# Performance work log

Hardware: AMD Instinct MI355X
Metric: run time of the kernel (lower is better)

## Reference

```python
import jax, jax.numpy as jnp
import numpy as np

NSAMPLE = 1024   # FPS centroids S
NGROUP = 32      # neighbors per ball K
RADIUS = 0.2


def _sqdist(a, b):
    # a: [B,S,3], b: [B,N,3] -> [B,S,N] squared euclidean distances
    return (jnp.sum(a * a, -1)[:, :, None]
            + jnp.sum(b * b, -1)[:, None, :]
            - 2.0 * jnp.einsum('bsc,bnc->bsn', a, b))


def farthest_point_sample(xyz, npoint):
    # xyz: [B,N,3] -> indices [B,npoint]. Deterministic start at index 0
    # (torch version randomizes the first centroid).
    B, N, _ = xyz.shape

    def step(carry, _):
        distance, farthest = carry
        centroid = jnp.take_along_axis(xyz, farthest[:, None, None], axis=1)  # [B,1,3]
        d = jnp.sum((xyz - centroid) ** 2, -1)                                 # [B,N]
        distance = jnp.minimum(distance, d)
        new_far = jnp.argmax(distance, -1).astype(jnp.int32)
        return (distance, new_far), farthest

    init = (jnp.full((B, N), 1e10, xyz.dtype), jnp.zeros((B,), jnp.int32))
    _, cents = jax.lax.scan(step, init, None, length=npoint)  # [npoint,B]
    return cents.T  # [B,npoint]


def query_ball_point(radius, nsample, xyz, new_xyz):
    # xyz: [B,N,3], new_xyz: [B,S,3] -> int idx [B,S,nsample]
    B, N, _ = xyz.shape
    sqr = _sqdist(new_xyz, xyz)                       # [B,S,N]
    idx = jnp.broadcast_to(jnp.arange(N, dtype=jnp.int32), sqr.shape)
    idx = jnp.where(sqr > radius * radius, N, idx)    # invalid -> sentinel N
    idx = jnp.sort(idx, axis=-1)[:, :, :nsample]      # smallest valid indices first
    first = idx[:, :, :1]
    idx = jnp.where(idx == N, first, idx)             # pad with first neighbor
    return idx.astype(jnp.int32)


def _gather_points(points, idx):
    # points: [B,N,C], idx: [B,S,K] -> [B,S,K,C]
    return jax.vmap(lambda p, i: p[i])(points, idx)


def setup_inputs() -> dict:
    key = jax.random.key(0)
    ks = jax.random.split(key, 8)
    B, N, D = 16, 8192, 64
    xyz = jax.random.uniform(ks[0], (B, N, 3), dtype=jnp.float32)
    points_fea = jax.random.normal(ks[1], (B, N, D), dtype=jnp.float32)
    s = 0.05
    W1 = jax.random.normal(ks[2], (67, 64), dtype=jnp.float32) * s
    b1 = jnp.zeros((64,), jnp.float32)
    W2 = jax.random.normal(ks[3], (64, 128), dtype=jnp.float32) * s
    b2 = jnp.zeros((128,), jnp.float32)
    W3 = jax.random.normal(ks[4], (128, 256), dtype=jnp.float32) * s
    b3 = jnp.zeros((256,), jnp.float32)
    return {"xyz": xyz, "points_fea": points_fea, "W1": W1, "b1": b1,
            "W2": W2, "b2": b2, "W3": W3, "b3": b3}


def reference(xyz, points_fea, W1, b1, W2, b2, W3, b3):
    # --- sample_and_group (fps + ball query) ---
    fps_idx = farthest_point_sample(xyz, NSAMPLE)                       # [B,S]
    sampled_xyz = jnp.take_along_axis(xyz, fps_idx[..., None], axis=1)  # [B,S,3]
    grouped_idx = query_ball_point(RADIUS, NGROUP, xyz, sampled_xyz)    # [B,S,K]
    grouped_xyz = _gather_points(xyz, grouped_idx)                      # [B,S,K,3]
    rel = grouped_xyz - sampled_xyz[:, :, None, :]
    grouped_fea = _gather_points(points_fea, grouped_idx)               # [B,S,K,D]
    feats = jnp.concatenate([rel, grouped_fea], axis=-1)                # [B,S,K,3+D]
    # --- per-point MLP (Linear+ReLU x3) ---
    h = jax.nn.relu(feats @ W1 + b1)
    h = jax.nn.relu(h @ W2 + b2)
    h = jax.nn.relu(h @ W3 + b3)                                        # [B,S,K,256]
    # --- max-pool over neighbors ---
    out = jnp.max(h, axis=2)                                            # [B,S,256]
    return sampled_xyz, out
```

## Files before the change

### kernel.cpp

```cpp
#include <hip/hip_runtime.h>
#include <hip/hip_bf16.h>

#define N_PTS 8192
#define NSAMP 1024
#define NGRP  32

typedef __attribute__((ext_vector_type(8))) short bf16x8;
typedef __attribute__((ext_vector_type(4))) float f32x4;

static __device__ inline unsigned short f2bf(float f) {
  __hip_bfloat16 h = __float2bfloat16(f);
  return __builtin_bit_cast(unsigned short, h);
}

#define DPP_MAXSTEP(r, ctrl)                                                  \
  r = fmaxf(r, __int_as_float(__builtin_amdgcn_update_dpp(                    \
          __float_as_int(r), __float_as_int(r), (ctrl), 0xf, 0xf, false)))

__global__
__attribute__((amdgpu_flat_work_group_size(512, 512)))
__attribute__((amdgpu_waves_per_eu(2, 2)))
void fps_kernel(
    const float* __restrict__ xyz, float* __restrict__ out_sampled)
{
  #pragma clang fp contract(off)
  const int b = blockIdx.x;
  const int t = threadIdx.x;
  const float* bx = xyz + (size_t)b * N_PTS * 3;

  float px[16], py[16], pz[16], dist[16];
  {
    const float4* src = (const float4*)(bx + t * 48);
    float4 v0 = src[0], v1 = src[1], v2 = src[2];
    float4 v3 = src[3], v4 = src[4], v5 = src[5];
    float4 v6 = src[6], v7 = src[7], v8 = src[8];
    float4 v9 = src[9], v10 = src[10], v11 = src[11];
    px[ 0]=v0.x; py[ 0]=v0.y; pz[ 0]=v0.z;
    px[ 1]=v0.w; py[ 1]=v1.x; pz[ 1]=v1.y;
    px[ 2]=v1.z; py[ 2]=v1.w; pz[ 2]=v2.x;
    px[ 3]=v2.y; py[ 3]=v2.z; pz[ 3]=v2.w;
    px[ 4]=v3.x; py[ 4]=v3.y; pz[ 4]=v3.z;
    px[ 5]=v3.w; py[ 5]=v4.x; pz[ 5]=v4.y;
    px[ 6]=v4.z; py[ 6]=v4.w; pz[ 6]=v5.x;
    px[ 7]=v5.y; py[ 7]=v5.z; pz[ 7]=v5.w;
    px[ 8]=v6.x; py[ 8]=v6.y; pz[ 8]=v6.z;
    px[ 9]=v6.w; py[ 9]=v7.x; pz[ 9]=v7.y;
    px[10]=v7.z; py[10]=v7.w; pz[10]=v8.x;
    px[11]=v8.y; py[11]=v8.z; pz[11]=v8.w;
    px[12]=v9.x; py[12]=v9.y; pz[12]=v9.z;
    px[13]=v9.w; py[13]=v10.x; pz[13]=v10.y;
    px[14]=v10.z; py[14]=v10.w; pz[14]=v11.x;
    px[15]=v11.y; py[15]=v11.z; pz[15]=v11.w;
  }
  #pragma unroll
  for (int r = 0; r < 16; ++r) dist[r] = 10000000000.0f;

  __shared__ uint2 part[2][8];
  __shared__ float out_lds[NSAMP * 3];

  const int lane = t & 63;
  const int wv   = t >> 6;

  float cx = bx[0], cy = bx[1], cz = bx[2];

  for (int it = 0; it < NSAMP; ++it) {
    if (t == 0) {
      out_lds[it * 3 + 0] = cx;
      out_lds[it * 3 + 1] = cy;
      out_lds[it * 3 + 2] = cz;
    }

    float bv = -1.0f;
    #pragma unroll
    for (int r = 0; r < 16; ++r) {
      float dx = px[r] - cx;
      float dy = py[r] - cy;
      float dz = pz[r] - cz;
      float d  = fmaf(dz, dz, fmaf(dy, dy, dx * dx));
      float nd = fminf(dist[r], d);
      dist[r] = nd;
      bv = fmaxf(bv, nd);
    }
    int bi = t * 16 + 15;
    #pragma unroll
    for (int r = 14; r >= 0; --r) bi = (dist[r] == bv) ? (t * 16 + r) : bi;

    float rmax = bv;
    DPP_MAXSTEP(rmax, 0x111);
    DPP_MAXSTEP(rmax, 0x112);
    DPP_MAXSTEP(rmax, 0x114);
    DPP_MAXSTEP(rmax, 0x118);
    DPP_MAXSTEP(rmax, 0x142);
    DPP_MAXSTEP(rmax, 0x143);
    float vmax = __int_as_float(
        __builtin_amdgcn_readlane(__float_as_int(rmax), 63));

    unsigned long long m = __ballot(bv == vmax);
    int L = __ffsll((long long)m) - 1;
    int widx = __builtin_amdgcn_readlane(bi, L);

    const int slot = it & 1;
    if (lane == 0) part[slot][wv] = make_uint2(__float_as_uint(vmax), (unsigned)widx);
    __syncthreads();

    const uint4* pp = (const uint4*)&part[slot][0];
    uint4 p0 = pp[0], p1 = pp[1], p2 = pp[2], p3 = pp[3];
    float v = __uint_as_float(p0.x); unsigned f = p0.y;
    float w1v = __uint_as_float(p0.z);
    if (w1v > v) { v = w1v; f = p0.w; }
    float w2v = __uint_as_float(p1.x);
    if (w2v > v) { v = w2v; f = p1.y; }
    float w3v = __uint_as_float(p1.z);
    if (w3v > v) { v = w3v; f = p1.w; }
    float w4v = __uint_as_float(p2.x);
    if (w4v > v) { v = w4v; f = p2.y; }
    float w5v = __uint_as_float(p2.z);
    if (w5v > v) { v = w5v; f = p2.w; }
    float w6v = __uint_as_float(p3.x);
    if (w6v > v) { v = w6v; f = p3.y; }
    float w7v = __uint_as_float(p3.z);
    if (w7v > v) { v = w7v; f = p3.w; }

    cx = bx[f * 3 + 0];
    cy = bx[f * 3 + 1];
    cz = bx[f * 3 + 2];
  }

  __syncthreads();
  float* ob = out_sampled + (size_t)b * NSAMP * 3;
  for (int i = t; i < NSAMP * 3; i += 512) ob[i] = out_lds[i];
}

__global__ __launch_bounds__(256) void ball_kernel(
    const float* __restrict__ xyz, const float* __restrict__ sampled,
    int* __restrict__ gidx)
{
  #pragma clang fp contract(off)
  const float R2 = (float)(0.2 * 0.2);
  int gt = blockIdx.x * 256 + threadIdx.x;
  int w = gt >> 6;
  int lane = gt & 63;
  const int b = w >> 10;
  const float* cp = sampled + (size_t)w * 3;
  float cx = cp[0], cy = cp[1], cz = cp[2];
  float na = ((cx * cx) + (cy * cy)) + (cz * cz);
  const float* bx = xyz + (size_t)b * N_PTS * 3;
  int* out = gidx + (size_t)w * NGRP;

  int cnt = 0;
  int first = 0;
  for (int base = 0; base < N_PTS && cnt < NGRP; base += 64) {
    int p = base + lane;
    float x = bx[p * 3 + 0];
    float y = bx[p * 3 + 1];
    float z = bx[p * 3 + 2];
    float nb  = ((x * x) + (y * y)) + (z * z);
    float dot = fmaf(cz, z, fmaf(cy, y, cx * x));
    float sq  = (na + nb) - (2.0f * dot);
    bool inr = !(sq > R2);
    unsigned long long m = __ballot(inr);
    if (cnt == 0 && m != 0ull) first = base + (__ffsll(m) - 1);
    int before = __popcll(m & ((1ull << lane) - 1ull));
    int pos = cnt + before;
    if (inr && pos < NGRP) out[pos] = p;
    cnt += __popcll(m);
  }
  if (cnt < NGRP) {
    int q = cnt + lane;
    if (q < NGRP) out[q] = first;
  }
}

__global__ __launch_bounds__(256) void prep_w_kernel(
    const float* __restrict__ W1, const float* __restrict__ W2,
    const float* __restrict__ W3, unsigned short* __restrict__ wf1,
    unsigned short* __restrict__ wf2, unsigned short* __restrict__ wf3)
{
  int tid = blockIdx.x * 256 + threadIdx.x;
  int rec = tid >> 6, lane = tid & 63;
  if (rec >= 92) return;
  const float* W; unsigned short* dst; int N, K, ksteps, rl;
  if (rec < 12)      { W = W1; dst = wf1; N = 64;  K = 67;  ksteps = 3; rl = rec; }
  else if (rec < 28) { W = W2; dst = wf2; N = 128; K = 64;  ksteps = 2; rl = rec - 12; }
  else               { W = W3; dst = wf3; N = 256; K = 128; ksteps = 4; rl = rec - 28; }
  int nt = rl / ksteps, ks = rl - nt * ksteps;
  int n  = nt * 16 + (lane & 15);
  int kb = ks * 32 + (lane >> 4) * 8;
  unsigned short v[8] __attribute__((aligned(16)));
  #pragma unroll
  for (int j = 0; j < 8; ++j) {
    int k = kb + j;
    v[j] = f2bf((k < K) ? W[k * N + n] : 0.0f);
  }
  *(uint4*)(dst + ((size_t)rl * 64 + lane) * 8) = *(const uint4*)v;
}

__global__ __launch_bounds__(256, 4) void mlp_mfma_kernel(
    const float* __restrict__ xyz, const float* __restrict__ fea,
    const float* __restrict__ sampled, const int* __restrict__ gidx,
    const unsigned short* __restrict__ wf1, const unsigned short* __restrict__ wf2,
    const unsigned short* __restrict__ wf3, const float* __restrict__ b1,
    const float* __restrict__ b2, const float* __restrict__ b3,
    float* __restrict__ out)
{
  __shared__ __align__(16) unsigned short fT[32][104];
  __shared__ __align__(16) unsigned short h1[32][72];
  __shared__ __align__(16) unsigned short h2[32][136];
  __shared__ float pmax[8][256];
  __shared__ int   sidx[32];
  __shared__ float sc[4];

  const int bs = blockIdx.x;
  const int b  = bs >> 10;
  const int t  = threadIdx.x;
  const int w    = t >> 6;
  const int lane = t & 63;
  const int quad = lane >> 4;
  const int ncol = lane & 15;

  if (t < 32) sidx[t] = gidx[(size_t)bs * 32 + t];
  if (t < 3)  sc[t] = sampled[(size_t)bs * 3 + t];
  __syncthreads();

  {
    const int pt = t >> 3, c0 = t & 7;
    const int p = sidx[pt];
    const float* xp = xyz + ((size_t)b * N_PTS + p) * 3;
    const float* fp = fea + ((size_t)b * N_PTS + p) * 64;
    for (int c = c0; c < 96; c += 8) {
      float v = (c < 3) ? (xp[c] - sc[c]) : (c < 67 ? fp[c - 3] : 0.0f);
      fT[pt][c] = f2bf(v);
    }
  }
  __syncthreads();

  #pragma unroll
  for (int q2 = 0; q2 < 2; ++q2) {
    const int tid = w * 2 + q2, mt = tid & 1, nt = tid >> 1;
    float bb = b1[nt * 16 + ncol];
    f32x4 acc = {bb, bb, bb, bb};
    #pragma unroll
    for (int ks = 0; ks < 3; ++ks) {
      bf16x8 a = *(const bf16x8*)&fT[mt * 16 + ncol][ks * 32 + quad * 8];
      bf16x8 bf = *(const bf16x8*)(wf1 + ((size_t)(nt * 3 + ks) * 64 + lane) * 8);
      acc = __builtin_amdgcn_mfma_f32_16x16x32_bf16(a, bf, acc, 0, 0, 0);
    }
    #pragma unroll
    for (int r = 0; r < 4; ++r)
      h1[mt * 16 + quad * 4 + r][nt * 16 + ncol] = f2bf(fmaxf(acc[r], 0.0f));
  }
  __syncthreads();

  #pragma unroll
  for (int q2 = 0; q2 < 4; ++q2) {
    const int tid = w * 4 + q2, mt = tid & 1, nt = tid >> 1;
    float bb = b2[nt * 16 + ncol];
    f32x4 acc = {bb, bb, bb, bb};
    #pragma unroll
    for (int ks = 0; ks < 2; ++ks) {
      bf16x8 a = *(const bf16x8*)&h1[mt * 16 + ncol][ks * 32 + quad * 8];
      bf16x8 bf = *(const bf16x8*)(wf2 + ((size_t)(nt * 2 + ks) * 64 + lane) * 8);
      acc = __builtin_amdgcn_mfma_f32_16x16x32_bf16(a, bf, acc, 0, 0, 0);
    }
    #pragma unroll
    for (int r = 0; r < 4; ++r)
      h2[mt * 16 + quad * 4 + r][nt * 16 + ncol] = f2bf(fmaxf(acc[r], 0.0f));
  }
  __syncthreads();

  #pragma unroll
  for (int q2 = 0; q2 < 8; ++q2) {
    const int tid = w * 8 + q2, mt = tid & 1, nt = tid >> 1;
    float bb = b3[nt * 16 + ncol];
    f32x4 acc = {bb, bb, bb, bb};
    #pragma unroll
    for (int ks = 0; ks < 4; ++ks) {
      bf16x8 a = *(const bf16x8*)&h2[mt * 16 + ncol][ks * 32 + quad * 8];
      bf16x8 bf = *(const bf16x8*)(wf3 + ((size_t)(nt * 4 + ks) * 64 + lane) * 8);
      acc = __builtin_amdgcn_mfma_f32_16x16x32_bf16(a, bf, acc, 0, 0, 0);
    }
    float mx = fmaxf(fmaxf(acc[0], acc[1]), fmaxf(acc[2], acc[3]));
    pmax[mt * 4 + quad][nt * 16 + ncol] = mx;
  }
  __syncthreads();

  {
    float v = pmax[0][t];
    #pragma unroll
    for (int s = 1; s < 8; ++s) v = fmaxf(v, pmax[s][t]);
    out[(size_t)bs * 256 + t] = fmaxf(v, 0.0f);
  }
}

extern "C" void kernel_launch(void* const* d_in, const int* in_sizes, int n_in,
                              void* d_out, int out_size, void* d_ws, size_t ws_size,
                              hipStream_t stream) {
  const float* xyz = (const float*)d_in[0];
  const float* fea = (const float*)d_in[1];
  const float* W1  = (const float*)d_in[2];
  const float* b1  = (const float*)d_in[3];
  const float* W2  = (const float*)d_in[4];
  const float* b2  = (const float*)d_in[5];
  const float* W3  = (const float*)d_in[6];
  const float* b3  = (const float*)d_in[7];

  float* outp    = (float*)d_out;
  float* sampled = outp;
  float* mlp_out = outp + 16 * 1024 * 3;
  int*   gidx    = (int*)d_ws;
  unsigned short* wf1 = (unsigned short*)((char*)d_ws + (2u << 20));
  unsigned short* wf2 = wf1 + (size_t)12 * 64 * 8;
  unsigned short* wf3 = wf2 + (size_t)16 * 64 * 8;

  fps_kernel<<<16, 512, 0, stream>>>(xyz, sampled);
  prep_w_kernel<<<23, 256, 0, stream>>>(W1, W2, W3, wf1, wf2, wf3);
  ball_kernel<<<4096, 256, 0, stream>>>(xyz, sampled, gidx);
  mlp_mfma_kernel<<<16384, 256, 0, stream>>>(xyz, fea, sampled, gidx,
                                             wf1, wf2, wf3, b1, b2, b3, mlp_out);
}
```

Before: 1.096 ms.

## Fuse FPS, ball query and MLP into one persistent producer-consumer kernel

Merges the three kernels into one persistent launch. Sixteen blocks run farthest point sampling and publish centroids in chunks of 64 through atomic counters, while the remaining blocks pull tasks from an atomic work queue, spin-wait until their centroid is ready, then do the ball query in one wave and the MLP. The aim is to overlap the serial FPS phase with grouping and MLP work and to drop the gidx round trip through global memory and the separate launches. In exchange it relies on co-residency of all 256 blocks to avoid deadlock, adds spin-wait and atomic overhead, and leaves only 240 consumer blocks of 512 threads doing the MLP.

```diff
diff --git a/kernel.cpp b/kernel.cpp
--- a/kernel.cpp
+++ b/kernel.cpp
@@ -4,6 +4,7 @@
 #define N_PTS 8192
 #define NSAMP 1024
 #define NGRP  32
+#define NTASK (16 * NSAMP)
 
 typedef __attribute__((ext_vector_type(8))) short bf16x8;
 typedef __attribute__((ext_vector_type(4))) float f32x4;
@@ -16,160 +17,6 @@
 #define DPP_MAXSTEP(r, ctrl)                                                  \
   r = fmaxf(r, __int_as_float(__builtin_amdgcn_update_dpp(                    \
           __float_as_int(r), __float_as_int(r), (ctrl), 0xf, 0xf, false)))
-
-__global__
-__attribute__((amdgpu_flat_work_group_size(512, 512)))
-__attribute__((amdgpu_waves_per_eu(2, 2)))
-void fps_kernel(
-    const float* __restrict__ xyz, float* __restrict__ out_sampled)
-{
-  #pragma clang fp contract(off)
-  const int b = blockIdx.x;
-  const int t = threadIdx.x;
-  const float* bx = xyz + (size_t)b * N_PTS * 3;
-
-  float px[16], py[16], pz[16], dist[16];
-  {
-    const float4* src = (const float4*)(bx + t * 48);
-    float4 v0 = src[0], v1 = src[1], v2 = src[2];
-    float4 v3 = src[3], v4 = src[4], v5 = src[5];
-    float4 v6 = src[6], v7 = src[7], v8 = src[8];
-    float4 v9 = src[9], v10 = src[10], v11 = src[11];
-    px[ 0]=v0.x; py[ 0]=v0.y; pz[ 0]=v0.z;
-    px[ 1]=v0.w; py[ 1]=v1.x; pz[ 1]=v1.y;
-    px[ 2]=v1.z; py[ 2]=v1.w; pz[ 2]=v2.x;
-    px[ 3]=v2.y; py[ 3]=v2.z; pz[ 3]=v2.w;
-    px[ 4]=v3.x; py[ 4]=v3.y; pz[ 4]=v3.z;
-    px[ 5]=v3.w; py[ 5]=v4.x; pz[ 5]=v4.y;
-    px[ 6]=v4.z; py[ 6]=v4.w; pz[ 6]=v5.x;
-    px[ 7]=v5.y; py[ 7]=v5.z; pz[ 7]=v5.w;
-    px[ 8]=v6.x; py[ 8]=v6.y; pz[ 8]=v6.z;
-    px[ 9]=v6.w; py[ 9]=v7.x; pz[ 9]=v7.y;
-    px[10]=v7.z; py[10]=v7.w; pz[10]=v8.x;
-    px[11]=v8.y; py[11]=v8.z; pz[11]=v8.w;
-    px[12]=v9.x; py[12]=v9.y; pz[12]=v9.z;
-    px[13]=v9.w; py[13]=v10.x; pz[13]=v10.y;
-    px[14]=v10.z; py[14]=v10.w; pz[14]=v11.x;
-    px[15]=v11.y; py[15]=v11.z; pz[15]=v11.w;
-  }
-  #pragma unroll
-  for (int r = 0; r < 16; ++r) dist[r] = 10000000000.0f;
-
-  __shared__ uint2 part[2][8];
-  __shared__ float out_lds[NSAMP * 3];
-
-  const int lane = t & 63;
-  const int wv   = t >> 6;
-
-  float cx = bx[0], cy = bx[1], cz = bx[2];
-
-  for (int it = 0; it < NSAMP; ++it) {
-    if (t == 0) {
-      out_lds[it * 3 + 0] = cx;
-      out_lds[it * 3 + 1] = cy;
-      out_lds[it * 3 + 2] = cz;
-    }
-
-    float bv = -1.0f;
-    #pragma unroll
-    for (int r = 0; r < 16; ++r) {
-      float dx = px[r] - cx;
-      float dy = py[r] - cy;
-      float dz = pz[r] - cz;
-      float d  = fmaf(dz, dz, fmaf(dy, dy, dx * dx));
-      float nd = fminf(dist[r], d);
-      dist[r] = nd;
-      bv = fmaxf(bv, nd);
-    }
-    int bi = t * 16 + 15;
-    #pragma unroll
-    for (int r = 14; r >= 0; --r) bi = (dist[r] == bv) ? (t * 16 + r) : bi;
-
-    float rmax = bv;
-    DPP_MAXSTEP(rmax, 0x111);
-    DPP_MAXSTEP(rmax, 0x112);
-    DPP_MAXSTEP(rmax, 0x114);
-    DPP_MAXSTEP(rmax, 0x118);
-    DPP_MAXSTEP(rmax, 0x142);
-    DPP_MAXSTEP(rmax, 0x143);
-    float vmax = __int_as_float(
-        __builtin_amdgcn_readlane(__float_as_int(rmax), 63));
-
-    unsigned long long m = __ballot(bv == vmax);
-    int L = __ffsll((long long)m) - 1;
-    int widx = __builtin_amdgcn_readlane(bi, L);
-
-    const int slot = it & 1;
-    if (lane == 0) part[slot][wv] = make_uint2(__float_as_uint(vmax), (unsigned)widx);
-    __syncthreads();
-
-    const uint4* pp = (const uint4*)&part[slot][0];
-    uint4 p0 = pp[0], p1 = pp[1], p2 = pp[2], p3 = pp[3];
-    float v = __uint_as_float(p0.x); unsigned f = p0.y;
-    float w1v = __uint_as_float(p0.z);
-    if (w1v > v) { v = w1v; f = p0.w; }
-    float w2v = __uint_as_float(p1.x);
-    if (w2v > v) { v = w2v; f = p1.y; }
-    float w3v = __uint_as_float(p1.z);
-    if (w3v > v) { v = w3v; f = p1.w; }
-    float w4v = __uint_as_float(p2.x);
-    if (w4v > v) { v = w4v; f = p2.y; }
-    float w5v = __uint_as_float(p2.z);
-    if (w5v > v) { v = w5v; f = p2.w; }
-    float w6v = __uint_as_float(p3.x);
-    if (w6v > v) { v = w6v; f = p3.y; }
-    float w7v = __uint_as_float(p3.z);
-    if (w7v > v) { v = w7v; f = p3.w; }
-
-    cx = bx[f * 3 + 0];
-    cy = bx[f * 3 + 1];
-    cz = bx[f * 3 + 2];
-  }
-
-  __syncthreads();
-  float* ob = out_sampled + (size_t)b * NSAMP * 3;
-  for (int i = t; i < NSAMP * 3; i += 512) ob[i] = out_lds[i];
-}
-
-__global__ __launch_bounds__(256) void ball_kernel(
-    const float* __restrict__ xyz, const float* __restrict__ sampled,
-    int* __restrict__ gidx)
-{
-  #pragma clang fp contract(off)
-  const float R2 = (float)(0.2 * 0.2);
-  int gt = blockIdx.x * 256 + threadIdx.x;
-  int w = gt >> 6;
-  int lane = gt & 63;
-  const int b = w >> 10;
-  const float* cp = sampled + (size_t)w * 3;
-  float cx = cp[0], cy = cp[1], cz = cp[2];
-  float na = ((cx * cx) + (cy * cy)) + (cz * cz);
-  const float* bx = xyz + (size_t)b * N_PTS * 3;
-  int* out = gidx + (size_t)w * NGRP;
-
-  int cnt = 0;
-  int first = 0;
-  for (int base = 0; base < N_PTS && cnt < NGRP; base += 64) {
-    int p = base + lane;
-    float x = bx[p * 3 + 0];
-    float y = bx[p * 3 + 1];
-    float z = bx[p * 3 + 2];
-    float nb  = ((x * x) + (y * y)) + (z * z);
-    float dot = fmaf(cz, z, fmaf(cy, y, cx * x));
-    float sq  = (na + nb) - (2.0f * dot);
-    bool inr = !(sq > R2);
-    unsigned long long m = __ballot(inr);
-    if (cnt == 0 && m != 0ull) first = base + (__ffsll(m) - 1);
-    int before = __popcll(m & ((1ull << lane) - 1ull));
-    int pos = cnt + before;
-    if (inr && pos < NGRP) out[pos] = p;
-    cnt += __popcll(m);
-  }
-  if (cnt < NGRP) {
-    int q = cnt + lane;
-    if (q < NGRP) out[q] = first;
-  }
-}
 
 __global__ __launch_bounds__(256) void prep_w_kernel(
     const float* __restrict__ W1, const float* __restrict__ W2,
@@ -195,100 +42,264 @@
   *(uint4*)(dst + ((size_t)rl * 64 + lane) * 8) = *(const uint4*)v;
 }
 
-__global__ __launch_bounds__(256, 4) void mlp_mfma_kernel(
+__global__
+__attribute__((amdgpu_flat_work_group_size(512, 512)))
+__attribute__((amdgpu_waves_per_eu(2, 2)))
+void fused_kernel(
     const float* __restrict__ xyz, const float* __restrict__ fea,
-    const float* __restrict__ sampled, const int* __restrict__ gidx,
+    float* __restrict__ out_sampled, float* __restrict__ out_mlp,
     const unsigned short* __restrict__ wf1, const unsigned short* __restrict__ wf2,
     const unsigned short* __restrict__ wf3, const float* __restrict__ b1,
     const float* __restrict__ b2, const float* __restrict__ b3,
-    float* __restrict__ out)
+    unsigned* __restrict__ ctrl)
 {
+  #pragma clang fp contract(off)
+  const int blk = blockIdx.x;
+  const int t = threadIdx.x;
+
+  if (blk < 16) {
+    const int b = blk;
+    const float* bx = xyz + (size_t)b * N_PTS * 3;
+
+    float px[16], py[16], pz[16], dist[16];
+    {
+      const float4* src = (const float4*)(bx + t * 48);
+      float4 v0 = src[0], v1 = src[1], v2 = src[2];
+      float4 v3 = src[3], v4 = src[4], v5 = src[5];
+      float4 v6 = src[6], v7 = src[7], v8 = src[8];
+      float4 v9 = src[9], v10 = src[10], v11 = src[11];
+      px[ 0]=v0.x; py[ 0]=v0.y; pz[ 0]=v0.z;
+      px[ 1]=v0.w; py[ 1]=v1.x; pz[ 1]=v1.y;
+      px[ 2]=v1.z; py[ 2]=v1.w; pz[ 2]=v2.x;
+      px[ 3]=v2.y; py[ 3]=v2.z; pz[ 3]=v2.w;
+      px[ 4]=v3.x; py[ 4]=v3.y; pz[ 4]=v3.z;
+      px[ 5]=v3.w; py[ 5]=v4.x; pz[ 5]=v4.y;
+      px[ 6]=v4.z; py[ 6]=v4.w; pz[ 6]=v5.x;
+      px[ 7]=v5.y; py[ 7]=v5.z; pz[ 7]=v5.w;
+      px[ 8]=v6.x; py[ 8]=v6.y; pz[ 8]=v6.z;
+      px[ 9]=v6.w; py[ 9]=v7.x; pz[ 9]=v7.y;
+      px[10]=v7.z; py[10]=v7.w; pz[10]=v8.x;
+      px[11]=v8.y; py[11]=v8.z; pz[11]=v8.w;
+      px[12]=v9.x; py[12]=v9.y; pz[12]=v9.z;
+      px[13]=v9.w; py[13]=v10.x; pz[13]=v10.y;
+      px[14]=v10.z; py[14]=v10.w; pz[14]=v11.x;
+      px[15]=v11.y; py[15]=v11.z; pz[15]=v11.w;
+    }
+    #pragma unroll
+    for (int r = 0; r < 16; ++r) dist[r] = 10000000000.0f;
+
+    __shared__ uint2 part[2][8];
+    __shared__ float out_lds[NSAMP * 3];
+
+    const int lane = t & 63;
+    const int wv   = t >> 6;
+
+    float cx = bx[0], cy = bx[1], cz = bx[2];
+
+    for (int it = 0; it < NSAMP; ++it) {
+      if (t == 0) {
+        out_lds[it * 3 + 0] = cx;
+        out_lds[it * 3 + 1] = cy;
+        out_lds[it * 3 + 2] = cz;
+      }
+
+      float bv = -1.0f;
+      #pragma unroll
+      for (int r = 0; r < 16; ++r) {
+        float dx = px[r] - cx;
+        float dy = py[r] - cy;
+        float dz = pz[r] - cz;
+        float d  = fmaf(dz, dz, fmaf(dy, dy, dx * dx));
+        float nd = fminf(dist[r], d);
+        dist[r] = nd;
+        bv = fmaxf(bv, nd);
+      }
+      int bi = t * 16 + 15;
+      #pragma unroll
+      for (int r = 14; r >= 0; --r) bi = (dist[r] == bv) ? (t * 16 + r) : bi;
+
+      float rmax = bv;
+      DPP_MAXSTEP(rmax, 0x111);
+      DPP_MAXSTEP(rmax, 0x112);
+      DPP_MAXSTEP(rmax, 0x114);
+      DPP_MAXSTEP(rmax, 0x118);
+      DPP_MAXSTEP(rmax, 0x142);
+      DPP_MAXSTEP(rmax, 0x143);
+      float vmax = __int_as_float(
+          __builtin_amdgcn_readlane(__float_as_int(rmax), 63));
+
+      unsigned long long m = __ballot(bv == vmax);
+      int L = __ffsll((long long)m) - 1;
+      int widx = __builtin_amdgcn_readlane(bi, L);
+
+      const int slot = it & 1;
+      if (lane == 0) part[slot][wv] = make_uint2(__float_as_uint(vmax), (unsigned)widx);
+      __syncthreads();
+
+      const uint4* pp = (const uint4*)&part[slot][0];
+      uint4 p0 = pp[0], p1 = pp[1], p2 = pp[2], p3 = pp[3];
+      float v = __uint_as_float(p0.x); unsigned f = p0.y;
+      float w1v = __uint_as_float(p0.z);
+      if (w1v > v) { v = w1v; f = p0.w; }
+      float w2v = __uint_as_float(p1.x);
+      if (w2v > v) { v = w2v; f = p1.y; }
+      float w3v = __uint_as_float(p1.z);
+      if (w3v > v) { v = w3v; f = p1.w; }
+      float w4v = __uint_as_float(p2.x);
+      if (w4v > v) { v = w4v; f = p2.y; }
+      float w5v = __uint_as_float(p2.z);
+      if (w5v > v) { v = w5v; f = p2.w; }
+      float w6v = __uint_as_float(p3.x);
+      if (w6v > v) { v = w6v; f = p3.y; }
+      float w7v = __uint_as_float(p3.z);
+      if (w7v > v) { v = w7v; f = p3.w; }
+
+      cx = bx[f * 3 + 0];
+      cy = bx[f * 3 + 1];
+      cz = bx[f * 3 + 2];
+
+      if ((it & 63) == 63) {
+        const int c = it >> 6;
+        if (t < 192) {
+          float* ob = out_sampled + (size_t)b * NSAMP * 3;
+          ob[c * 192 + t] = out_lds[c * 192 + t];
+        }
+        __syncthreads();
+        if (t == 0)
+          __hip_atomic_fetch_add(&ctrl[1 + b], 64u, __ATOMIC_RELEASE,
+                                 __HIP_MEMORY_SCOPE_AGENT);
+      }
+    }
+    return;
+  }
+
   __shared__ __align__(16) unsigned short fT[32][104];
-  __shared__ __align__(16) unsigned short h1[32][72];
-  __shared__ __align__(16) unsigned short h2[32][136];
+  __shared__ __align__(16) unsigned short h1c[32][72];
+  __shared__ __align__(16) unsigned short h2c[32][136];
   __shared__ float pmax[8][256];
   __shared__ int   sidx[32];
-  __shared__ float sc[4];
-
-  const int bs = blockIdx.x;
-  const int b  = bs >> 10;
-  const int t  = threadIdx.x;
+  __shared__ float s_c[4];
+  __shared__ int   s_task;
+
   const int w    = t >> 6;
   const int lane = t & 63;
   const int quad = lane >> 4;
   const int ncol = lane & 15;
 
-  if (t < 32) sidx[t] = gidx[(size_t)bs * 32 + t];
-  if (t < 3)  sc[t] = sampled[(size_t)bs * 3 + t];
-  __syncthreads();
-
-  {
-    const int pt = t >> 3, c0 = t & 7;
-    const int p = sidx[pt];
-    const float* xp = xyz + ((size_t)b * N_PTS + p) * 3;
-    const float* fp = fea + ((size_t)b * N_PTS + p) * 64;
-    for (int c = c0; c < 96; c += 8) {
-      float v = (c < 3) ? (xp[c] - sc[c]) : (c < 67 ? fp[c - 3] : 0.0f);
-      fT[pt][c] = f2bf(v);
-    }
-  }
-  __syncthreads();
-
-  #pragma unroll
-  for (int q2 = 0; q2 < 2; ++q2) {
-    const int tid = w * 2 + q2, mt = tid & 1, nt = tid >> 1;
-    float bb = b1[nt * 16 + ncol];
-    f32x4 acc = {bb, bb, bb, bb};
+  for (;;) {
+    if (t == 0) s_task = (int)atomicAdd(&ctrl[0], 1u);
+    __syncthreads();
+    const int task = s_task;
+    if (task >= NTASK) break;
+    const int b = task & 15, idx = task >> 4;
+
+    if (t == 0) {
+      while ((int)__hip_atomic_load(&ctrl[1 + b], __ATOMIC_RELAXED,
+                                    __HIP_MEMORY_SCOPE_AGENT) <= idx)
+        __builtin_amdgcn_s_sleep(8);
+      (void)__hip_atomic_load(&ctrl[1 + b], __ATOMIC_ACQUIRE,
+                              __HIP_MEMORY_SCOPE_AGENT);
+      const float* cp = out_sampled + ((size_t)b * NSAMP + idx) * 3;
+      s_c[0] = cp[0]; s_c[1] = cp[1]; s_c[2] = cp[2];
+    }
+    __syncthreads();
+
+    if (w == 0) {
+      const float R2 = (float)(0.2 * 0.2);
+      float cx = s_c[0], cy = s_c[1], cz = s_c[2];
+      float na = ((cx * cx) + (cy * cy)) + (cz * cz);
+      const float* bx = xyz + (size_t)b * N_PTS * 3;
+      int cnt = 0, first = 0;
+      for (int base = 0; base < N_PTS && cnt < NGRP; base += 64) {
+        int p = base + lane;
+        float x = bx[p * 3 + 0];
+        float y = bx[p * 3 + 1];
+        float z = bx[p * 3 + 2];
+        float nb  = ((x * x) + (y * y)) + (z * z);
+        float dot = fmaf(cz, z, fmaf(cy, y, cx * x));
+        float sq  = (na + nb) - (2.0f * dot);
+        bool inr = !(sq > R2);
+        unsigned long long mm = __ballot(inr);
+        if (cnt == 0 && mm != 0ull) first = base + (__ffsll((long long)mm) - 1);
+        int before = __popcll(mm & ((1ull << lane) - 1ull));
+        int pos = cnt + before;
+        if (inr && pos < NGRP) sidx[pos] = p;
+        cnt += __popcll(mm);
+      }
+      if (cnt < NGRP) { int q = cnt + lane; if (q < NGRP) sidx[q] = first; }
+    }
+    __syncthreads();
+
+    {
+      const int pt = t >> 4, c0 = t & 15;
+      const int p = sidx[pt];
+      const float* xp = xyz + ((size_t)b * N_PTS + p) * 3;
+      const float* fp = fea + ((size_t)b * N_PTS + p) * 64;
+      #pragma unroll
+      for (int c = c0; c < 96; c += 16) {
+        float v = (c < 3) ? (xp[c] - s_c[c]) : (c < 67 ? fp[c - 3] : 0.0f);
+        fT[pt][c] = f2bf(v);
+      }
+    }
+    __syncthreads();
+
+    {
+      const int mt = w & 1, nt = w >> 1;
+      float bb = b1[nt * 16 + ncol];
+      f32x4 acc = {bb, bb, bb, bb};
+      #pragma unroll
+      for (int ks = 0; ks < 3; ++ks) {
+        bf16x8 a = *(const bf16x8*)&fT[mt * 16 + ncol][ks * 32 + quad * 8];
+        bf16x8 bf = *(const bf16x8*)(wf1 + ((size_t)(nt * 3 + ks) * 64 + lane) * 8);
+        acc = __builtin_amdgcn_mfma_f32_16x16x32_bf16(a, bf, acc, 0, 0, 0);
+      }
+      #pragma unroll
+      for (int r = 0; r < 4; ++r)
+        h1c[mt * 16 + quad * 4 + r][nt * 16 + ncol] = f2bf(fmaxf(acc[r], 0.0f));
+    }
+    __syncthreads();
+
     #pragma unroll
-    for (int ks = 0; ks < 3; ++ks) {
-      bf16x8 a = *(const bf16x8*)&fT[mt * 16 + ncol][ks * 32 + quad * 8];
-      bf16x8 bf = *(const bf16x8*)(wf1 + ((size_t)(nt * 3 + ks) * 64 + lane) * 8);
-      acc = __builtin_amdgcn_mfma_f32_16x16x32_bf16(a, bf, acc, 0, 0, 0);
-    }
+    for (int q2 = 0; q2 < 2; ++q2) {
+      const int tid = w * 2 + q2, mt = tid & 1, nt = tid >> 1;
+      float bb = b2[nt * 16 + ncol];
+      f32x4 acc = {bb, bb, bb, bb};
+      #pragma unroll
+      for (int ks = 0; ks < 2; ++ks) {
+        bf16x8 a = *(const bf16x8*)&h1c[mt * 16 + ncol][ks * 32 + quad * 8];
+        bf16x8 bf = *(const bf16x8*)(wf2 + ((size_t)(nt * 2 + ks) * 64 + lane) * 8);
+        acc = __builtin_amdgcn_mfma_f32_16x16x32_bf16(a, bf, acc, 0, 0, 0);
+      }
+      #pragma unroll
+      for (int r = 0; r < 4; ++r)
+        h2c[mt * 16 + quad * 4 + r][nt * 16 + ncol] = f2bf(fmaxf(acc[r], 0.0f));
+    }
+    __syncthreads();
+
     #pragma unroll
-    for (int r = 0; r < 4; ++r)
-      h1[mt * 16 + quad * 4 + r][nt * 16 + ncol] = f2bf(fmaxf(acc[r], 0.0f));
-  }
-  __syncthreads();
-
-  #pragma unroll
-  for (int q2 = 0; q2 < 4; ++q2) {
-    const int tid = w * 4 + q2, mt = tid & 1, nt = tid >> 1;
-    float bb = b2[nt * 16 + ncol];
-    f32x4 acc = {bb, bb, bb, bb};
-    #pragma unroll
-    for (int ks = 0; ks < 2; ++ks) {
-      bf16x8 a = *(const bf16x8*)&h1[mt * 16 + ncol][ks * 32 + quad * 8];
-      bf16x8 bf = *(const bf16x8*)(wf2 + ((size_t)(nt * 2 + ks) * 64 + lane) * 8);
-      acc = __builtin_amdgcn_mfma_f32_16x16x32_bf16(a, bf, acc, 0, 0, 0);
-    }
-    #pragma unroll
-    for (int r = 0; r < 4; ++r)
-      h2[mt * 16 + quad * 4 + r][nt * 16 + ncol] = f2bf(fmaxf(acc[r], 0.0f));
-  }
-  __syncthreads();
-
-  #pragma unroll
-  for (int q2 = 0; q2 < 8; ++q2) {
-    const int tid = w * 8 + q2, mt = tid & 1, nt = tid >> 1;
-    float bb = b3[nt * 16 + ncol];
-    f32x4 acc = {bb, bb, bb, bb};
-    #pragma unroll
-    for (int ks = 0; ks < 4; ++ks) {
-      bf16x8 a = *(const bf16x8*)&h2[mt * 16 + ncol][ks * 32 + quad * 8];
-      bf16x8 bf = *(const bf16x8*)(wf3 + ((size_t)(nt * 4 + ks) * 64 + lane) * 8);
-      acc = __builtin_amdgcn_mfma_f32_16x16x32_bf16(a, bf, acc, 0, 0, 0);
-    }
-    float mx = fmaxf(fmaxf(acc[0], acc[1]), fmaxf(acc[2], acc[3]));
-    pmax[mt * 4 + quad][nt * 16 + ncol] = mx;
-  }
-  __syncthreads();
-
-  {
-    float v = pmax[0][t];
-    #pragma unroll
-    for (int s = 1; s < 8; ++s) v = fmaxf(v, pmax[s][t]);
-    out[(size_t)bs * 256 + t] = fmaxf(v, 0.0f);
+    for (int q2 = 0; q2 < 4; ++q2) {
+      const int tid = w * 4 + q2, mt = tid & 1, nt = tid >> 1;
+      float bb = b3[nt * 16 + ncol];
+      f32x4 acc = {bb, bb, bb, bb};
+      #pragma unroll
+      for (int ks = 0; ks < 4; ++ks) {
+        bf16x8 a = *(const bf16x8*)&h2c[mt * 16 + ncol][ks * 32 + quad * 8];
+        bf16x8 bf = *(const bf16x8*)(wf3 + ((size_t)(nt * 4 + ks) * 64 + lane) * 8);
+        acc = __builtin_amdgcn_mfma_f32_16x16x32_bf16(a, bf, acc, 0, 0, 0);
+      }
+      float mx = fmaxf(fmaxf(acc[0], acc[1]), fmaxf(acc[2], acc[3]));
+      pmax[mt * 4 + quad][nt * 16 + ncol] = mx;
+    }
+    __syncthreads();
+
+    if (t < 256) {
+      float v = pmax[0][t];
+      #pragma unroll
+      for (int s = 1; s < 8; ++s) v = fmaxf(v, pmax[s][t]);
+      out_mlp[((size_t)task) * 0 + ((size_t)((b << 10) + idx)) * 256 + t] =
+          fmaxf(v, 0.0f);
+    }
+    __syncthreads();
   }
 }
 
@@ -307,14 +318,14 @@
   float* outp    = (float*)d_out;
   float* sampled = outp;
   float* mlp_out = outp + 16 * 1024 * 3;
-  int*   gidx    = (int*)d_ws;
-  unsigned short* wf1 = (unsigned short*)((char*)d_ws + (2u << 20));
+
+  unsigned* ctrl = (unsigned*)d_ws;
+  unsigned short* wf1 = (unsigned short*)((char*)d_ws + 256);
   unsigned short* wf2 = wf1 + (size_t)12 * 64 * 8;
   unsigned short* wf3 = wf2 + (size_t)16 * 64 * 8;
 
-  fps_kernel<<<16, 512, 0, stream>>>(xyz, sampled);
+  hipMemsetAsync(ctrl, 0, 256, stream);
   prep_w_kernel<<<23, 256, 0, stream>>>(W1, W2, W3, wf1, wf2, wf3);
-  ball_kernel<<<4096, 256, 0, stream>>>(xyz, sampled, gidx);
-  mlp_mfma_kernel<<<16384, 256, 0, stream>>>(xyz, fea, sampled, gidx,
-                                             wf1, wf2, wf3, b1, b2, b3, mlp_out);
+  fused_kernel<<<256, 512, 0, stream>>>(xyz, fea, sampled, mlp_out,
+                                        wf1, wf2, wf3, b1, b2, b3, ctrl);
 }
```

Result: slower. 1.323 ms (+20.7%).
